# Performance work log

Hardware: AMD Instinct MI355X
Metric: run time of the kernel (lower is better)

The kernel has to match this reference:

```python
import jax, jax.numpy as jnp
import numpy as np

NUM_HEADS = 16

def setup_inputs() -> dict:
    key = jax.random.key(0)
    k1, k2, k3 = jax.random.split(key, 3)
    B, S, D = 4, 2048, 1024
    x = jax.random.normal(k1, (B, S, D), dtype=jnp.float32)
    w_qkv = jax.random.normal(k2, (D, 3 * D), dtype=jnp.float32) * (1.0 / np.sqrt(D))
    b_qkv = jnp.zeros((3 * D,), dtype=jnp.float32)
    w_out = jax.random.normal(k3, (D, D), dtype=jnp.float32) * (1.0 / np.sqrt(D))
    b_out = jnp.zeros((D,), dtype=jnp.float32)
    return {"x": x, "w_qkv": w_qkv, "b_qkv": b_qkv, "w_out": w_out, "b_out": b_out}

def reference(x, w_qkv, b_qkv, w_out, b_out):
    B, S, D = x.shape
    H = NUM_HEADS
    Dh = D // H
    # fused QKV projection: [B,S,3D]
    qkv = jnp.einsum('bsd,de->bse', x, w_qkv) + b_qkv
    q, k, v = jnp.split(qkv, 3, axis=-1)
    # separate heads -> [B,H,S,Dh]
    def heads(t):
        return t.reshape(B, S, H, Dh).transpose(0, 2, 1, 3)
    q, k, v = heads(q), heads(k), heads(v)
    # scaled dot-product attention (no mask, no dropout)
    scale = 1.0 / jnp.sqrt(jnp.asarray(Dh, dtype=x.dtype))
    attn = jnp.einsum('bhqd,bhkd->bhqk', q, k) * scale
    weights = jax.nn.softmax(attn, axis=-1)
    out = jnp.einsum('bhqk,bhkd->bhqd', weights, v)
    # combine heads -> [B,S,D], then output projection
    out = out.transpose(0, 2, 1, 3).reshape(B, S, D)
    return jnp.einsum('bsd,de->bse', out, w_out) + b_out
```

## Files before the change

### kernel.cpp

```cpp
#include <hip/hip_runtime.h>

typedef unsigned short u16;
typedef __attribute__((ext_vector_type(8))) short v8s;
typedef __attribute__((ext_vector_type(4))) short v4s;
typedef __attribute__((ext_vector_type(4))) float v4f;

#define MFMA32(a, b, c) __builtin_amdgcn_mfma_f32_16x16x32_bf16(a, b, c, 0, 0, 0)

#if __has_builtin(__builtin_amdgcn_mfma_f32_16x16x16bf16_1k)
static __device__ __forceinline__ v4f mfma16(v4s a, v4s b, v4f c) {
    return __builtin_amdgcn_mfma_f32_16x16x16bf16_1k(a, b, c, 0, 0, 0);
}
#else
static __device__ __forceinline__ v4f mfma16(v4s a, v4s b, v4f c) {
    v4s z = {0, 0, 0, 0};
    v8s a8 = __builtin_shufflevector(a, z, 0, 1, 2, 3, 4, 5, 6, 7);
    v8s b8 = __builtin_shufflevector(b, z, 0, 1, 2, 3, 4, 5, 6, 7);
    return MFMA32(a8, b8, c);
}
#endif

static __device__ __forceinline__ u16 f32_to_bf16(float f) {
    unsigned int u = __builtin_bit_cast(unsigned int, f);
    u += 0x7fffu + ((u >> 16) & 1u);
    return (u16)(u >> 16);
}

#if __has_builtin(__builtin_amdgcn_cvt_pk_bf16_f32)
typedef __attribute__((ext_vector_type(2))) __bf16 v2bf;
static __device__ __forceinline__ int cvt_pk2(float a, float b) {
    v2bf p = __builtin_amdgcn_cvt_pk_bf16_f32(a, b);
    return __builtin_bit_cast(int, p);
}
#else
static __device__ __forceinline__ int cvt_pk2(float a, float b) {
    return (int)f32_to_bf16(a) | ((int)f32_to_bf16(b) << 16);
}
#endif
static __device__ __forceinline__ v4s pack4(float a, float b, float c, float d) {
    typedef __attribute__((ext_vector_type(2))) int v2i;
    v2i p = {cvt_pk2(a, b), cvt_pk2(c, d)};
    return __builtin_bit_cast(v4s, p);
}
static __device__ __forceinline__ v8s cvt8(v4f lo, v4f hi) {
    typedef __attribute__((ext_vector_type(4))) int v4i;
    v4i p = {cvt_pk2(lo[0], lo[1]), cvt_pk2(lo[2], lo[3]),
             cvt_pk2(hi[0], hi[1]), cvt_pk2(hi[2], hi[3])};
    return __builtin_bit_cast(v8s, p);
}

__global__ void cast_f32_bf16(const float* __restrict__ in,
                              u16* __restrict__ out, int n8) {
    const int i = blockIdx.x * blockDim.x + threadIdx.x;
    if (i < n8) {
        v4f lo = ((const v4f*)in)[2 * i];
        v4f hi = ((const v4f*)in)[2 * i + 1];
        ((v8s*)out)[i] = cvt8(lo, hi);
    }
}

__global__ void transpose_f32_bf16(const float* __restrict__ in,
                                   u16* __restrict__ out, int R, int C) {
    __shared__ u16 t[32][33];
    const int tid = threadIdx.x;
    const int tx = tid & 31, ty = tid >> 5;
    const int c0 = blockIdx.x * 32, r0 = blockIdx.y * 32;
#pragma unroll
    for (int i = 0; i < 32; i += 8)
        t[ty + i][tx] = f32_to_bf16(in[(size_t)(r0 + ty + i) * C + c0 + tx]);
    __syncthreads();
#pragma unroll
    for (int i = 0; i < 32; i += 8)
        out[(size_t)(c0 + ty + i) * R + r0 + tx] = t[tx][ty + i];
}

template <int CMODE>
__global__ __launch_bounds__(256)
void gemm_bt(const u16* __restrict__ Au, int lda,
             const u16* __restrict__ Bt, int ldb,
             const float* __restrict__ bias,
             void* __restrict__ Cq, u16* __restrict__ Kb, u16* __restrict__ VtG,
             int ldc, int K) {
    __shared__ __align__(16) u16 As[128 * 72];
    __shared__ __align__(16) u16 Bs[128 * 72];

    const int tid  = threadIdx.x;
    const int wid  = tid >> 6;
    const int lane = tid & 63;
    const int l15  = lane & 15;
    const int quad = lane >> 4;
    const int bm = blockIdx.y * 128;
    const int bn = blockIdx.x * 128;
    const int wm = (wid & 1) * 64;
    const int wn = (wid >> 1) * 64;

    const int sr = tid >> 3;
    const int sg = (tid & 7) * 8;

    v4f acc[4][4];
#pragma unroll
    for (int i = 0; i < 4; i++)
#pragma unroll
        for (int j = 0; j < 4; j++) acc[i][j] = (v4f)0.f;

    for (int kb = 0; kb < K; kb += 64) {
        v8s a[4], b[4];
#pragma unroll
        for (int i = 0; i < 4; i++) {
            const int row = sr + i * 32;
            a[i] = *(const v8s*)(Au + (size_t)(bm + row) * lda + kb + sg);
            b[i] = *(const v8s*)(Bt + (size_t)(bn + row) * ldb + kb + sg);
        }
        __syncthreads();
#pragma unroll
        for (int i = 0; i < 4; i++) {
            const int row = sr + i * 32;
            *(v8s*)&As[row * 72 + sg] = a[i];
            *(v8s*)&Bs[row * 72 + sg] = b[i];
        }
        __syncthreads();

        v8s af[2][4], bf[2][4];
#pragma unroll
        for (int ko = 0; ko < 2; ko++) {
#pragma unroll
            for (int mt = 0; mt < 4; mt++)
                af[ko][mt] = *(const v8s*)&As[(wm + mt * 16 + l15) * 72 + ko * 32 + quad * 8];
#pragma unroll
            for (int nt = 0; nt < 4; nt++)
                bf[ko][nt] = *(const v8s*)&Bs[(wn + nt * 16 + l15) * 72 + ko * 32 + quad * 8];
        }
#pragma unroll
        for (int ko = 0; ko < 2; ko++)
#pragma unroll
            for (int mt = 0; mt < 4; mt++)
#pragma unroll
                for (int nt = 0; nt < 4; nt++)
                    acc[mt][nt] = MFMA32(af[ko][mt], bf[ko][nt], acc[mt][nt]);
    }

#pragma unroll
    for (int nt = 0; nt < 4; nt++) {
        const int n = bn + wn + nt * 16 + l15;
        const float bv = bias[n];
#pragma unroll
        for (int mt = 0; mt < 4; mt++) {
#pragma unroll
            for (int r = 0; r < 4; r++) {
                const int m = bm + wm + mt * 16 + quad * 4 + r;
                const float val = acc[mt][nt][r] + bv;
                if (CMODE == 1) {
                    ((float*)Cq)[(size_t)m * ldc + n] = val;
                } else {
                    const u16 o = f32_to_bf16(val);
                    const int region = n >> 10, nl = n & 1023;
                    if (region == 0) {
                        ((u16*)Cq)[(size_t)m * 1024 + nl] = o;
                    } else if (region == 1) {
                        Kb[(size_t)m * 1024 + nl] = o;
                    } else {
                        const int h = nl >> 6, dh = nl & 63;
                        const int b = m >> 11, s = m & 2047;
                        VtG[((size_t)((b * 16 + h) * 64 + dh)) * 2048 + s] = o;
                    }
                }
            }
        }
    }
}

__global__ __launch_bounds__(256)
void attn_fused(u16* __restrict__ Qb, const u16* __restrict__ Kb,
                const u16* __restrict__ VtG) {
    __shared__ __align__(16) u16 Ks[64 * 72];
    __shared__ __align__(16) u16 Vs[64 * 72];

    const int tid  = threadIdx.x;
    const int wid  = tid >> 6;
    const int lane = tid & 63;
    const int l15  = lane & 15;
    const int quad = lane >> 4;
    const int qt = blockIdx.x;
    const int h  = blockIdx.y;
    const int bz = blockIdx.z;

    const size_t qbase = (size_t)bz * 2048 * 1024;
    const int q0 = qt * 128 + wid * 32;

    v8s aq[2][2];
#pragma unroll
    for (int qh = 0; qh < 2; qh++) {
        const u16* qrow = Qb + qbase + (size_t)(q0 + qh * 16 + l15) * 1024 + h * 64 + quad * 8;
        aq[qh][0] = *(const v8s*)qrow;
        aq[qh][1] = *(const v8s*)(qrow + 32);
    }

    float lrow[2] = {0.f, 0.f};
    v4f accO[2][4];
#pragma unroll
    for (int qh = 0; qh < 2; qh++)
#pragma unroll
        for (int c = 0; c < 4; c++) accO[qh][c] = (v4f)0.f;

    const int sr = tid >> 3;
    const int sg = (tid & 7) * 8;
    const float SC = 0.18033688f;

    const u16* kpb = Kb + qbase + h * 64;
    const u16* vpb = VtG + (size_t)((bz * 16 + h) * 64) * 2048;

    for (int kt = 0; kt < 32; kt++) {
        const v8s k0 = *(const v8s*)(kpb + (size_t)(kt * 64 + sr) * 1024 + sg);
        const v8s k1 = *(const v8s*)(kpb + (size_t)(kt * 64 + sr + 32) * 1024 + sg);
        const v8s v0 = *(const v8s*)(vpb + (size_t)sr * 2048 + kt * 64 + sg);
        const v8s v1 = *(const v8s*)(vpb + (size_t)(sr + 32) * 2048 + kt * 64 + sg);
        __syncthreads();
        *(v8s*)&Ks[sr * 72 + sg]        = k0;
        *(v8s*)&Ks[(sr + 32) * 72 + sg] = k1;
        *(v8s*)&Vs[sr * 72 + sg]        = v0;
        *(v8s*)&Vs[(sr + 32) * 72 + sg] = v1;
        __syncthreads();

#pragma unroll
        for (int kc = 0; kc < 4; kc++) {
            const v8s kf0 = *(const v8s*)&Ks[(kc * 16 + l15) * 72 + quad * 8];
            const v8s kf1 = *(const v8s*)&Ks[(kc * 16 + l15) * 72 + 32 + quad * 8];
            v4s vf[4];
#pragma unroll
            for (int c = 0; c < 4; c++)
                vf[c] = *(const v4s*)&Vs[(c * 16 + l15) * 72 + kc * 16 + quad * 4];

#pragma unroll
            for (int qh = 0; qh < 2; qh++) {
                v4f st = (v4f)0.f;
                st = MFMA32(kf0, aq[qh][0], st);
                st = MFMA32(kf1, aq[qh][1], st);
                const float p0 = exp2f(st[0] * SC);
                const float p1 = exp2f(st[1] * SC);
                const float p2 = exp2f(st[2] * SC);
                const float p3 = exp2f(st[3] * SC);
                lrow[qh] += (p0 + p1) + (p2 + p3);
                const v4s pk = pack4(p0, p1, p2, p3);
#pragma unroll
                for (int c = 0; c < 4; c++)
                    accO[qh][c] = mfma16(vf[c], pk, accO[qh][c]);
            }
        }
    }

#pragma unroll
    for (int qh = 0; qh < 2; qh++) {
        lrow[qh] += __shfl_xor(lrow[qh], 16);
        lrow[qh] += __shfl_xor(lrow[qh], 32);
    }

#pragma unroll
    for (int qh = 0; qh < 2; qh++) {
        const int q = q0 + qh * 16 + l15;
        const float inv = 1.f / lrow[qh];
#pragma unroll
        for (int c = 0; c < 4; c++) {
            const v4s o = pack4(accO[qh][c][0] * inv, accO[qh][c][1] * inv,
                                accO[qh][c][2] * inv, accO[qh][c][3] * inv);
            *(v4s*)&Qb[qbase + (size_t)q * 1024 + h * 64 + c * 16 + quad * 4] = o;
        }
    }
}

extern "C" void kernel_launch(void* const* d_in, const int* in_sizes, int n_in,
                              void* d_out, int out_size, void* d_ws, size_t ws_size,
                              hipStream_t stream) {
    (void)in_sizes; (void)n_in; (void)out_size;
    const float* x    = (const float*)d_in[0];
    const float* wqkv = (const float*)d_in[1];
    const float* bqkv = (const float*)d_in[2];
    const float* wout = (const float*)d_in[3];
    const float* bout = (const float*)d_in[4];
    float* outp = (float*)d_out;

    char* ws = (char*)d_ws;
    const size_t BIG = 58720256;

    if (ws_size >= BIG || ws_size == 0) {
        u16* Qb    = (u16*)(ws);
        u16* Kb    = (u16*)(ws + 16777216);
        u16* VtG   = (u16*)(ws + 33554432);
        u16* wqkvT = (u16*)(ws + 50331648);
        u16* woutT = (u16*)(ws + 56623104);
        u16* xb    = (u16*)outp;

        transpose_f32_bf16<<<dim3(96, 32), 256, 0, stream>>>(wqkv, wqkvT, 1024, 3072);
        transpose_f32_bf16<<<dim3(32, 32), 256, 0, stream>>>(wout, woutT, 1024, 1024);
        cast_f32_bf16<<<4096, 256, 0, stream>>>(x, xb, 1048576);
        gemm_bt<2><<<dim3(24, 64), 256, 0, stream>>>(
            xb, 1024, wqkvT, 1024, bqkv, Qb, Kb, VtG, 0, 1024);
        attn_fused<<<dim3(16, 16, 4), 256, 0, stream>>>(Qb, Kb, VtG);
        gemm_bt<1><<<dim3(8, 64), 256, 0, stream>>>(
            Qb, 1024, woutT, 1024, bout, outp, nullptr, nullptr, 1024, 1024);
    } else {
        u16* wqkvT = (u16*)(ws);
        u16* woutT = (u16*)(ws + 6291456);
        u16* Qb    = (u16*)(ws + 8388608);
        u16* Kb    = (u16*)(ws + 12582912);
        u16* VtG   = (u16*)(ws + 16777216);

        transpose_f32_bf16<<<dim3(96, 32), 256, 0, stream>>>(wqkv, wqkvT, 1024, 3072);
        transpose_f32_bf16<<<dim3(32, 32), 256, 0, stream>>>(wout, woutT, 1024, 1024);
        for (int b = 0; b < 4; b++) {
            const float* xf = x + (size_t)b * 2048 * 1024;
            float* ob = outp + (size_t)b * 2048 * 1024;
            u16* xb = (u16*)((char*)ob + 4194304);
            cast_f32_bf16<<<1024, 256, 0, stream>>>(xf, xb, 262144);
            gemm_bt<2><<<dim3(24, 16), 256, 0, stream>>>(
                xb, 1024, wqkvT, 1024, bqkv, Qb, Kb, VtG, 0, 1024);
            attn_fused<<<dim3(16, 16, 1), 256, 0, stream>>>(Qb, Kb, VtG);
            gemm_bt<1><<<dim3(8, 16), 256, 0, stream>>>(
                Qb, 1024, woutT, 1024, bout, ob, nullptr, nullptr, 1024, 1024);
        }
    }
}
```

Measured before the change: 359.9 us.

## Load GEMM tiles directly into LDS with global_load_lds and shrink K-step

The QKV and output-projection GEMM now uses the direct global-to-LDS load builtin (16-byte per lane) instead of loading into registers and then storing to shared memory. To fit the per-wave contiguous layout the builtin needs, the K-step is halved from 64 to 32 and the padded LDS stride is dropped. This removes register staging and ds_write traffic, but doubles the number of barriers per K. The unpadded 32-element rows can also cause LDS bank conflicts on the fragment reads.

```diff
diff --git a/kernel.cpp b/kernel.cpp
--- a/kernel.cpp
+++ b/kernel.cpp
@@ -47,6 +47,12 @@
     v4i p = {cvt_pk2(lo[0], lo[1]), cvt_pk2(lo[2], lo[3]),
              cvt_pk2(hi[0], hi[1]), cvt_pk2(hi[2], hi[3])};
     return __builtin_bit_cast(v8s, p);
+}
+
+static __device__ __forceinline__ void gload16(const void* g, void* l) {
+    __builtin_amdgcn_global_load_lds(
+        (const __attribute__((address_space(1))) unsigned int*)g,
+        (__attribute__((address_space(3))) unsigned int*)l, 16, 0, 0);
 }
 
 __global__ void cast_f32_bf16(const float* __restrict__ in,
@@ -81,8 +87,8 @@
              const float* __restrict__ bias,
              void* __restrict__ Cq, u16* __restrict__ Kb, u16* __restrict__ VtG,
              int ldc, int K) {
-    __shared__ __align__(16) u16 As[128 * 72];
-    __shared__ __align__(16) u16 Bs[128 * 72];
+    __shared__ __align__(16) u16 As[128 * 32];
+    __shared__ __align__(16) u16 Bs[128 * 32];
 
     const int tid  = threadIdx.x;
     const int wid  = tid >> 6;
@@ -94,8 +100,8 @@
     const int wm = (wid & 1) * 64;
     const int wn = (wid >> 1) * 64;
 
-    const int sr = tid >> 3;
-    const int sg = (tid & 7) * 8;
+    const int drow = wid * 16 + (lane >> 2);
+    const int dcol = (lane & 3) * 8;
 
     v4f acc[4][4];
 #pragma unroll
@@ -103,40 +109,26 @@
 #pragma unroll
         for (int j = 0; j < 4; j++) acc[i][j] = (v4f)0.f;
 
-    for (int kb = 0; kb < K; kb += 64) {
-        v8s a[4], b[4];
-#pragma unroll
-        for (int i = 0; i < 4; i++) {
-            const int row = sr + i * 32;
-            a[i] = *(const v8s*)(Au + (size_t)(bm + row) * lda + kb + sg);
-            b[i] = *(const v8s*)(Bt + (size_t)(bn + row) * ldb + kb + sg);
-        }
+    for (int kb = 0; kb < K; kb += 32) {
         __syncthreads();
-#pragma unroll
-        for (int i = 0; i < 4; i++) {
-            const int row = sr + i * 32;
-            *(v8s*)&As[row * 72 + sg] = a[i];
-            *(v8s*)&Bs[row * 72 + sg] = b[i];
-        }
+        gload16(Au + (size_t)(bm + drow) * lda + kb + dcol,      &As[drow * 32 + dcol]);
+        gload16(Au + (size_t)(bm + 64 + drow) * lda + kb + dcol, &As[(drow + 64) * 32 + dcol]);
+        gload16(Bt + (size_t)(bn + drow) * ldb + kb + dcol,      &Bs[drow * 32 + dcol]);
+        gload16(Bt + (size_t)(bn + 64 + drow) * ldb + kb + dcol, &Bs[(drow + 64) * 32 + dcol]);
         __syncthreads();
 
-        v8s af[2][4], bf[2][4];
-#pragma unroll
-        for (int ko = 0; ko < 2; ko++) {
-#pragma unroll
-            for (int mt = 0; mt < 4; mt++)
-                af[ko][mt] = *(const v8s*)&As[(wm + mt * 16 + l15) * 72 + ko * 32 + quad * 8];
+        v8s af[4], bf[4];
+#pragma unroll
+        for (int mt = 0; mt < 4; mt++)
+            af[mt] = *(const v8s*)&As[(wm + mt * 16 + l15) * 32 + quad * 8];
+#pragma unroll
+        for (int nt = 0; nt < 4; nt++)
+            bf[nt] = *(const v8s*)&Bs[(wn + nt * 16 + l15) * 32 + quad * 8];
+#pragma unroll
+        for (int mt = 0; mt < 4; mt++)
 #pragma unroll
             for (int nt = 0; nt < 4; nt++)
-                bf[ko][nt] = *(const v8s*)&Bs[(wn + nt * 16 + l15) * 72 + ko * 32 + quad * 8];
-        }
-#pragma unroll
-        for (int ko = 0; ko < 2; ko++)
-#pragma unroll
-            for (int mt = 0; mt < 4; mt++)
-#pragma unroll
-                for (int nt = 0; nt < 4; nt++)
-                    acc[mt][nt] = MFMA32(af[ko][mt], bf[ko][nt], acc[mt][nt]);
+                acc[mt][nt] = MFMA32(af[mt], bf[nt], acc[mt][nt]);
     }
 
 #pragma unroll
```

After: 350.1 us. -2.7%, faster.
